# Kernel tuning notes

Measured on AMD Instinct MI355X. Metric: run time of the kernel, lower is better.

## Reference

```python
import jax, jax.numpy as jnp
import numpy as np

EPSILON = 1e-6
MINMAX_RATIO = 20 ** 0.5
N_NODES, N_EDGES = 60000, 240000
WIDTH, NUM_HEAD, DIM_HEAD = 256, 8, 32
WIDTH_NORM = NUM_HEAD * DIM_HEAD          # 256
WIDTH_ACT = NUM_HEAD * DIM_HEAD * 4       # 1024
EDGE_VOCAB, EDGE_FEATS = 16, 3


def _inv_softplus(y):
    return np.log(np.expm1(y))


def setup_inputs() -> dict:
    key = jax.random.key(0)
    ks = jax.random.split(key, 16)
    inp = {
        'x': jax.random.normal(ks[0], (N_NODES, WIDTH), jnp.float32),
        'deg': jax.random.randint(ks[1], (N_NODES,), 0, 6, jnp.int32),
        'edge_idx': jax.random.randint(ks[2], (2, N_EDGES), 0, N_NODES, jnp.int32),
        'edge_attr': jax.random.randint(ks[3], (N_EDGES, EDGE_FEATS), 0, EDGE_VOCAB, jnp.int32),
        'node_elec': jax.random.normal(ks[4], (N_NODES, 2), jnp.float32),
        # parameters (init scales per module code)
        'lora_down': jax.random.normal(ks[5], (WIDTH, DIM_HEAD)) / np.sqrt(WIDTH),
        # original init is zeros; small random values used so this path is exercised
        'lora_up': jax.random.normal(ks[6], (DIM_HEAD, WIDTH_NORM)) * 0.01,
        'emb_edge': jax.random.normal(ks[7], (EDGE_VOCAB, DIM_HEAD)) * (0.01 / np.sqrt(EDGE_FEATS)),
        'moa_w': jnp.zeros((2, DIM_HEAD), jnp.float32),
        'moa_s': jnp.tile(jnp.linspace(float(_inv_softplus(0.1)), float(_inv_softplus(10.0)), DIM_HEAD), (2, 1)),
        'elec_lin': jax.random.normal(ks[8], (2, DIM_HEAD)) * (0.01 / np.sqrt(2)),
        'emb_deg': jax.random.normal(ks[9], (6, WIDTH_NORM)) * 0.1,
        'lin_pre': jax.random.normal(ks[10], (WIDTH, WIDTH_NORM)) / np.sqrt(WIDTH),
        'gate_lin': jax.random.normal(ks[11], (WIDTH_NORM, WIDTH_NORM)) / np.sqrt(WIDTH_NORM),
        'gate_kernel': jax.random.normal(ks[12], (NUM_HEAD, DIM_HEAD, DIM_HEAD * 4)) / np.sqrt(DIM_HEAD),
        'value_lin': jax.random.normal(ks[13], (WIDTH_NORM, WIDTH_NORM)) / np.sqrt(WIDTH_NORM),
        'value_kernel': jax.random.normal(ks[14], (NUM_HEAD, DIM_HEAD, DIM_HEAD * 4)) / np.sqrt(DIM_HEAD),
        'act_bias': jnp.full((WIDTH_ACT,), float(_inv_softplus(0.5)), jnp.float32),
        'post_kernel': jax.random.normal(ks[15], (NUM_HEAD, DIM_HEAD * 4, DIM_HEAD)) / np.sqrt(DIM_HEAD * 4),
    }
    return inp


def _clip_with_grad(x, lo, hi):
    return jax.lax.stop_gradient(jnp.clip(x, lo, hi) - x) + x


def _group_linear(x, lin_kernel, head_kernel, norm_bias=None):
    H, D, F = head_kernel.shape
    xx = (x @ lin_kernel).reshape(*x.shape[:-1], H, D)
    xx = xx / jnp.sqrt(jnp.mean(jnp.square(xx), axis=-1, keepdims=True) + EPSILON)
    if norm_bias is not None:
        xx = (xx + norm_bias.reshape(xx.shape)) / 2 ** 0.5
    xx = jnp.einsum('nhd,hdf->nhf', xx, head_kernel)
    return xx.reshape(*x.shape[:-1], H * F)


def reference(x, deg, edge_idx, edge_attr, node_elec, lora_down, lora_up, emb_edge,
              moa_w, moa_s, elec_lin, emb_deg, lin_pre, gate_lin, gate_kernel,
              value_lin, value_kernel, act_bias, post_kernel):
    ei0, ei1 = edge_idx[0], edge_idx[1]
    # edge embedding: bond features + electronegativity difference (MoAct tanh mixture)
    diff = node_elec[ei0] - node_elec[ei1]                      # [E,2]
    w = jax.nn.softplus(moa_w)
    w = w / w.sum(axis=-1, keepdims=True)
    s = jax.nn.softplus(moa_s)
    moa_out = (jnp.tanh(diff[..., None] * s) * w).sum(-1)       # [E,2]
    emb = jnp.sum(emb_edge[edge_attr], axis=-2) + moa_out @ elec_lin  # [E,dim_head]
    # per-edge message with LoRA modulation, scatter-add to destination nodes
    msg = x[ei0] + x[ei1]                                       # [E,width]
    msg = msg @ lin_pre + ((msg @ lora_down) * emb) @ lora_up   # [E,width_norm]
    agg = jax.ops.segment_sum(msg, ei1, num_segments=x.shape[0])
    # gated post-block with degree-embedding gate bias
    gate_bias = emb_deg[deg]                                    # [N,width_norm]
    gg = _group_linear(agg, gate_lin, gate_kernel, gate_bias)   # [N,width_act]
    vv = _group_linear(agg, value_lin, value_kernel)
    a = jax.nn.softplus(gg + act_bias)
    a = _clip_with_grad(a, 1.0 / MINMAX_RATIO, MINMAX_RATIO)
    xx = (a * vv).reshape(agg.shape[0], NUM_HEAD, -1)           # [N,H,4*dim_head]
    xx = jnp.einsum('nhd,hdf->nhf', xx, post_kernel)
    return xx.reshape(agg.shape[0], -1)                         # [N,width_norm]
```

## Files before the change

kernel.cpp:

```cpp
#include <hip/hip_runtime.h>
#include <hip/hip_bf16.h>

typedef unsigned short u16;

#define NN 60000
#define NE 240000

typedef __attribute__((ext_vector_type(8))) short bfrag;
typedef __attribute__((ext_vector_type(4))) float ffrag;

__device__ __forceinline__ float bf2f(u16 u) {
    union { unsigned int i; float f; } v; v.i = ((unsigned int)u) << 16; return v.f;
}
__device__ __forceinline__ u16 f2bf(float f) {
    __hip_bfloat16 h = __float2bfloat16(f);
    return *reinterpret_cast<u16*>(&h);
}
__device__ __forceinline__ float softplusf(float x) {
    return fmaxf(x, 0.f) + log1pf(expf(-fabsf(x)));
}
__device__ __forceinline__ float fast_softplus(float x) {
    return __logf(1.f + __expf(x));
}
__device__ __forceinline__ float fast_sp_clip(float x) {
    float a = __logf(1.f + __expf(x));
    return fminf(fmaxf(a, 0.22360679774997896f), 4.47213595499957939f);
}
__device__ __forceinline__ float fast_tanh(float x) {
    float t = __expf(fminf(fmaxf(2.f * x, -30.f), 30.f));
    return (t - 1.f) * __builtin_amdgcn_rcpf(t + 1.f);
}
template<bool B>
__device__ __forceinline__ float LD(const void* p, int i) {
    if constexpr (B) return bf2f(((const u16*)p)[i]);
    else             return ((const float*)p)[i];
}
__device__ __forceinline__ bfrag ldfrag(const u16* p) {
    return *reinterpret_cast<const bfrag*>(p);
}
__device__ __forceinline__ ffrag MFMA(bfrag a, bfrag b, ffrag c) {
    return __builtin_amdgcn_mfma_f32_16x16x32_bf16(a, b, c, 0, 0, 0);
}

__global__ void detect_kernel(const u16* __restrict__ x, int* __restrict__ flag) {
    __shared__ int cnt;
    if (threadIdx.x == 0) cnt = 0;
    __syncthreads();
    int c = 0;
    for (int i = threadIdx.x; i < 2048; i += 256) {
        u16 w = x[2 * i];
        int e = (w >> 7) & 0xFF;
        if (e >= 112 && e <= 143) c++;
    }
    atomicAdd(&cnt, c);
    __syncthreads();
    if (threadIdx.x == 0) *flag = (cnt > 1024) ? 1 : 0;
}

template<bool B>
__device__ void prep_body(const void* gate_lin, const void* value_lin,
    const void* lin_pre, const void* lora_down, const void* lora_up,
    const void* gate_kernel, const void* value_kernel, const void* post_kernel,
    u16* gT, u16* vT, u16* lpT, u16* ldT, u16* luT, u16* gkT, u16* vkT, u16* pkT,
    int tid, int stride)
{
    for (int i = tid; i < 65536; i += stride) {
        int n = i >> 8, k = i & 255;
        gT[i]  = f2bf(LD<B>(gate_lin,  k * 256 + n));
        vT[i]  = f2bf(LD<B>(value_lin, k * 256 + n));
        lpT[i] = f2bf(LD<B>(lin_pre,   k * 256 + n));
    }
    for (int i = tid; i < 8192; i += stride) {
        { int n = i >> 8, k = i & 255; ldT[i] = f2bf(LD<B>(lora_down, k * 32 + n)); }
        { int n = i >> 5, k = i & 31;  luT[i] = f2bf(LD<B>(lora_up,   k * 256 + n)); }
    }
    for (int i = tid; i < 32768; i += stride) {
        { int hf = i >> 5, d = i & 31, h = hf >> 7, f = hf & 127;
          gkT[i] = f2bf(LD<B>(gate_kernel,  h * 4096 + d * 128 + f));
          vkT[i] = f2bf(LD<B>(value_kernel, h * 4096 + d * 128 + f)); }
        { int hd = i >> 7, f = i & 127, h = hd >> 5, d2 = hd & 31;
          pkT[i] = f2bf(LD<B>(post_kernel, h * 4096 + f * 32 + d2)); }
    }
}
__global__ void prep_kernel(const void* gate_lin, const void* value_lin,
    const void* lin_pre, const void* lora_down, const void* lora_up,
    const void* gate_kernel, const void* value_kernel, const void* post_kernel,
    u16* gT, u16* vT, u16* lpT, u16* ldT, u16* luT, u16* gkT, u16* vkT, u16* pkT,
    const int* flag)
{
    int tid = blockIdx.x * blockDim.x + threadIdx.x;
    int stride = gridDim.x * blockDim.x;
    if (*flag) prep_body<true >(gate_lin, value_lin, lin_pre, lora_down, lora_up,
        gate_kernel, value_kernel, post_kernel, gT, vT, lpT, ldT, luT, gkT, vkT, pkT, tid, stride);
    else       prep_body<false>(gate_lin, value_lin, lin_pre, lora_down, lora_up,
        gate_kernel, value_kernel, post_kernel, gT, vT, lpT, ldT, luT, gkT, vkT, pkT, tid, stride);
}


struct PreSmem { __align__(16) u16 xB[64][264]; };

template<bool B>
__device__ void pre_body(PreSmem& sm, const void* x, const u16* ldT,
                         u16* xd, int blk, int j)
{
    const int w = j >> 6, quad = (j >> 4) & 3, l15 = j & 15;
    {
        int row = j >> 2, seg = j & 3, c0 = seg * 64;
        int gr = blk * 64 + row;
        if (gr < NN) {
            if constexpr (B) {
                const u16* xp = (const u16*)x + (size_t)gr * 256 + c0;
                for (int cc = 0; cc < 64; cc += 8)
                    *reinterpret_cast<bfrag*>(&sm.xB[row][c0 + cc]) = ldfrag(xp + cc);
            } else {
                const float* xp = (const float*)x + (size_t)gr * 256 + c0;
                for (int cc = 0; cc < 64; cc += 8) {
                    float4 v0 = *(const float4*)(xp + cc);
                    float4 v1 = *(const float4*)(xp + cc + 4);
                    bfrag o;
                    o[0] = (short)f2bf(v0.x); o[1] = (short)f2bf(v0.y);
                    o[2] = (short)f2bf(v0.z); o[3] = (short)f2bf(v0.w);
                    o[4] = (short)f2bf(v1.x); o[5] = (short)f2bf(v1.y);
                    o[6] = (short)f2bf(v1.z); o[7] = (short)f2bf(v1.w);
                    *reinterpret_cast<bfrag*>(&sm.xB[row][c0 + cc]) = o;
                }
            }
        } else {
            bfrag z = {0,0,0,0,0,0,0,0};
            for (int cc = 0; cc < 64; cc += 8)
                *reinterpret_cast<bfrag*>(&sm.xB[row][c0 + cc]) = z;
        }
    }
    __syncthreads();
    const int r0 = w * 16;
    bfrag A[8];
    #pragma unroll
    for (int kt = 0; kt < 8; kt++)
        A[kt] = ldfrag(&sm.xB[r0 + l15][kt * 32 + quad * 8]);

    #pragma unroll
    for (int t = 0; t < 2; t++) {
        int n0 = t * 16;
        ffrag acc = {0.f, 0.f, 0.f, 0.f};
        #pragma unroll
        for (int kt = 0; kt < 8; kt++)
            acc = MFMA(A[kt], ldfrag(ldT + (n0 + l15) * 256 + kt * 32 + quad * 8), acc);
        #pragma unroll
        for (int r = 0; r < 4; r++) {
            int gr = blk * 64 + r0 + quad * 4 + r;
            if (gr < NN) xd[(size_t)gr * 32 + n0 + l15] = f2bf(acc[r]);
        }
    }
}
__global__ __launch_bounds__(256) void pre_kernel(const void* x, const u16* ldT,
    u16* xd, const int* flag)
{
    __shared__ PreSmem sm;
    const int j = threadIdx.x, blk = blockIdx.x;
    if (*flag) pre_body<true >(sm, x, ldT, xd, blk, j);
    else       pre_body<false>(sm, x, ldT, xd, blk, j);
}

__global__ __launch_bounds__(256) void hist_kernel(const int* __restrict__ edge_idx,
                                                   int* __restrict__ cnt)
{
    int e = blockIdx.x * blockDim.x + threadIdx.x;
    int stride = gridDim.x * blockDim.x;
    for (; e < NE; e += stride) atomicAdd(&cnt[edge_idx[NE + e]], 1);
}

__global__ __launch_bounds__(256) void scanA_kernel(const int* __restrict__ cnt,
                                                    int* __restrict__ bsum)
{
    __shared__ int sd[256];
    int b = blockIdx.x, j = threadIdx.x;
    int base = b * 1024 + j * 4;
    int s = 0;
    #pragma unroll
    for (int k = 0; k < 4; k++) { int i = base + k; if (i < NN) s += cnt[i]; }
    sd[j] = s; __syncthreads();
    for (int st = 128; st > 0; st >>= 1) {
        if (j < st) sd[j] += sd[j + st];
        __syncthreads();
    }
    if (j == 0) bsum[b] = sd[0];
}

__global__ __launch_bounds__(256) void scanB_kernel(const int* __restrict__ cnt,
    const int* __restrict__ bsum, int* __restrict__ off, int* __restrict__ cur)
{
    __shared__ int sd[256];
    int b = blockIdx.x, j = threadIdx.x;
    int pre = 0;
    for (int k = 0; k < b; k++) pre += bsum[k];
    int base = b * 1024 + j * 4;
    int c[4]; int tsum = 0;
    #pragma unroll
    for (int k = 0; k < 4; k++) { int i = base + k; c[k] = (i < NN) ? cnt[i] : 0; tsum += c[k]; }
    sd[j] = tsum; __syncthreads();
    for (int st = 1; st < 256; st <<= 1) {
        int v = (j >= st) ? sd[j - st] : 0;
        __syncthreads();
        sd[j] += v;
        __syncthreads();
    }
    int excl = sd[j] - tsum;
    int run = pre + excl;
    #pragma unroll
    for (int k = 0; k < 4; k++) {
        int i = base + k;
        if (i < NN) { off[i] = run; cur[i] = run; }
        run += c[k];
    }
}

struct EdgeWSmem {
    float wL[64], sL[64];
    float embT[512];
    float elT[64];
};

template<bool B>
__device__ void edgew_body(EdgeWSmem& sm, const int* edge_idx, const int* edge_attr,
    const void* node_elec, const void* emb_edge, const void* moa_w, const void* moa_s,
    const void* elec_lin, const u16* xd, u16* W, int* srcL, int* cur, int g, int j)
{
    if (j < 64) {
        int c = j >> 5;
        float sw = fast_softplus(LD<B>(moa_w, j));
        float tot = 0.f;
        #pragma unroll
        for (int d = 0; d < 32; d++) tot += fast_softplus(LD<B>(moa_w, c * 32 + d));
        sm.wL[j] = sw / tot;
        sm.sL[j] = fast_softplus(LD<B>(moa_s, j));
        sm.elT[j] = LD<B>(elec_lin, j);
    }
    for (int i = j; i < 512; i += 256) sm.embT[i] = LD<B>(emb_edge, i);
    __syncthreads();

    const int t = j & 3, s = j >> 2, e = g * 64 + s;
    const int a = edge_idx[e], b = edge_idx[NE + e];
    const int ch = t >> 1, dr = (t & 1) * 16;
    float df = LD<B>(node_elec, a * 2 + ch) - LD<B>(node_elec, b * 2 + ch);
    float part = 0.f;
    #pragma unroll
    for (int d = 0; d < 16; d++) {
        int dd = ch * 32 + dr + d;
        part += fast_tanh(df * sm.sL[dd]) * sm.wL[dd];
    }
    part += __shfl_xor(part, 1);
    int base = (j & 63) & ~3;
    float moa0 = __shfl(part, base + 0);
    float moa1 = __shfl(part, base + 2);

    int a0 = edge_attr[e * 3 + 0], a1 = edge_attr[e * 3 + 1], a2 = edge_attr[e * 3 + 2];
    int d0 = t * 8;
    bfrag va = ldfrag(xd + (size_t)a * 32 + d0);
    bfrag vb = ldfrag(xd + (size_t)b * 32 + d0);
    bfrag o;
    #pragma unroll
    for (int q = 0; q < 8; q++) {
        int d = d0 + q;
        float emb = sm.embT[a0 * 32 + d] + sm.embT[a1 * 32 + d] + sm.embT[a2 * 32 + d]
                  + moa0 * sm.elT[d] + moa1 * sm.elT[32 + d];
        o[q] = (short)f2bf((bf2f((u16)va[q]) + bf2f((u16)vb[q])) * emb);
    }
    int slot = 0;
    if (t == 0) slot = atomicAdd(&cur[b], 1);
    slot = __shfl(slot, base);
    if (t == 0) srcL[slot] = a;
    *reinterpret_cast<bfrag*>(W + (size_t)slot * 32 + d0) = o;
}

__global__ __launch_bounds__(256) void edgew_kernel(const int* edge_idx,
    const int* edge_attr, const void* node_elec, const void* emb_edge,
    const void* moa_w, const void* moa_s, const void* elec_lin,
    const u16* xd, u16* W, int* srcL, int* cur, const int* flag)
{
    __shared__ EdgeWSmem sm;
    const int j = threadIdx.x, g = blockIdx.x;
    if (*flag) edgew_body<true >(sm, edge_idx, edge_attr, node_elec, emb_edge,
                                 moa_w, moa_s, elec_lin, xd, W, srcL, cur, g, j);
    else       edgew_body<false>(sm, edge_idx, edge_attr, node_elec, emb_edge,
                                 moa_w, moa_s, elec_lin, xd, W, srcL, cur, g, j);
}

struct GatherSmem {
    int srcC[192];
    int offL[16], idgL[16];
};

template<bool B>
__device__ void gather_body(GatherSmem& sm, const void* x, const u16* Wb,
    const int* srcL, const int* off, const int* cnt,
    u16* S, u16* U, int blk, int j)
{
    const int n0g = blk * 16;
    int o0 = off[n0g];
    int eb = off[n0g + 15] + cnt[n0g + 15] - o0;
    if (j < 192 && j < eb) sm.srcC[j] = srcL[o0 + j];
    if (j < 16) { sm.offL[j] = off[n0g + j]; sm.idgL[j] = cnt[n0g + j]; }
    __syncthreads();

    const int s = j >> 4, dp = j & 15, c0 = dp * 16;
    const int o = sm.offL[s], dg = sm.idgL[s], base = o - o0;
    float acc[16];
    #pragma unroll
    for (int k = 0; k < 16; k++) acc[k] = 0.f;
    float u0 = 0.f, u1 = 0.f;

    if constexpr (B) {
        const u16* xp = (const u16*)x;
        bfrag pv0 = {0,0,0,0,0,0,0,0}, pv1 = {0,0,0,0,0,0,0,0};
        float pw0 = 0.f, pw1 = 0.f;
        if (dg > 0) {
            int src = (base < 192) ? sm.srcC[base] : srcL[o];
            const u16* xr = xp + (size_t)src * 256 + c0;
            pv0 = ldfrag(xr); pv1 = ldfrag(xr + 8);
            const u16* wr = Wb + (size_t)o * 32 + dp;
            pw0 = bf2f(wr[0]); pw1 = bf2f(wr[16]);
        }
        for (int i = 0; i < dg; i++) {
            bfrag v0 = pv0, v1 = pv1;
            float w0 = pw0, w1 = pw1;
            if (i + 1 < dg) {
                int idx = base + i + 1;
                int src = (idx < 192) ? sm.srcC[idx] : srcL[o + i + 1];
                const u16* xr = xp + (size_t)src * 256 + c0;
                pv0 = ldfrag(xr); pv1 = ldfrag(xr + 8);
                const u16* wr = Wb + (size_t)(o + i + 1) * 32 + dp;
                pw0 = bf2f(wr[0]); pw1 = bf2f(wr[16]);
            }
            u0 += w0; u1 += w1;
            #pragma unroll
            for (int q = 0; q < 8; q++) {
                acc[q]     += bf2f((u16)v0[q]);
                acc[q + 8] += bf2f((u16)v1[q]);
            }
        }
        {
            const u16* xr = xp + (size_t)(n0g + s) * 256 + c0;
            bfrag v0 = ldfrag(xr), v1 = ldfrag(xr + 8);
            float fd = (float)dg;
            #pragma unroll
            for (int q = 0; q < 8; q++) {
                acc[q]     = fmaf(fd, bf2f((u16)v0[q]), acc[q]);
                acc[q + 8] = fmaf(fd, bf2f((u16)v1[q]), acc[q + 8]);
            }
        }
    } else {
        const float* xp = (const float*)x;
        float4 p0 = {0,0,0,0}, p1 = {0,0,0,0}, p2 = {0,0,0,0}, p3 = {0,0,0,0};
        float pw0 = 0.f, pw1 = 0.f;
        if (dg > 0) {
            int src = (base < 192) ? sm.srcC[base] : srcL[o];
            const float* r = xp + (size_t)src * 256 + c0;
            p0 = *(const float4*)r;       p1 = *(const float4*)(r + 4);
            p2 = *(const float4*)(r + 8); p3 = *(const float4*)(r + 12);
            const u16* wr = Wb + (size_t)o * 32 + dp;
            pw0 = bf2f(wr[0]); pw1 = bf2f(wr[16]);
        }
        for (int i = 0; i < dg; i++) {
            float4 a0 = p0, a1 = p1, a2 = p2, a3 = p3;
            float w0 = pw0, w1 = pw1;
            if (i + 1 < dg) {
                int idx = base + i + 1;
                int src = (idx < 192) ? sm.srcC[idx] : srcL[o + i + 1];
                const float* r = xp + (size_t)src * 256 + c0;
                p0 = *(const float4*)r;       p1 = *(const float4*)(r + 4);
                p2 = *(const float4*)(r + 8); p3 = *(const float4*)(r + 12);
                const u16* wr = Wb + (size_t)(o + i + 1) * 32 + dp;
                pw0 = bf2f(wr[0]); pw1 = bf2f(wr[16]);
            }
            u0 += w0; u1 += w1;
            acc[0]  += a0.x; acc[1]  += a0.y; acc[2]  += a0.z; acc[3]  += a0.w;
            acc[4]  += a1.x; acc[5]  += a1.y; acc[6]  += a1.z; acc[7]  += a1.w;
            acc[8]  += a2.x; acc[9]  += a2.y; acc[10] += a2.z; acc[11] += a2.w;
            acc[12] += a3.x; acc[13] += a3.y; acc[14] += a3.z; acc[15] += a3.w;
        }
        {
            const float* r = xp + (size_t)(n0g + s) * 256 + c0;
            float4 a0 = *(const float4*)r,       a1 = *(const float4*)(r + 4);
            float4 a2 = *(const float4*)(r + 8), a3 = *(const float4*)(r + 12);
            float fd = (float)dg;
            acc[0]  = fmaf(fd, a0.x, acc[0]);  acc[1]  = fmaf(fd, a0.y, acc[1]);
            acc[2]  = fmaf(fd, a0.z, acc[2]);  acc[3]  = fmaf(fd, a0.w, acc[3]);
            acc[4]  = fmaf(fd, a1.x, acc[4]);  acc[5]  = fmaf(fd, a1.y, acc[5]);
            acc[6]  = fmaf(fd, a1.z, acc[6]);  acc[7]  = fmaf(fd, a1.w, acc[7]);
            acc[8]  = fmaf(fd, a2.x, acc[8]);  acc[9]  = fmaf(fd, a2.y, acc[9]);
            acc[10] = fmaf(fd, a2.z, acc[10]); acc[11] = fmaf(fd, a2.w, acc[11]);
            acc[12] = fmaf(fd, a3.x, acc[12]); acc[13] = fmaf(fd, a3.y, acc[13]);
            acc[14] = fmaf(fd, a3.z, acc[14]); acc[15] = fmaf(fd, a3.w, acc[15]);
        }
    }

    u16* Sp = S + (size_t)(n0g + s) * 256 + c0;
    #pragma unroll
    for (int cq = 0; cq < 16; cq += 2) {
        unsigned int pv = (unsigned int)f2bf(acc[cq]) | ((unsigned int)f2bf(acc[cq + 1]) << 16);
        *reinterpret_cast<unsigned int*>(Sp + cq) = pv;
    }
    U[(size_t)(n0g + s) * 32 + dp]      = f2bf(u0);
    U[(size_t)(n0g + s) * 32 + dp + 16] = f2bf(u1);
}

__global__ __launch_bounds__(256) void gather_kernel(const void* x, const u16* Wb,
    const int* srcL, const int* off, const int* cnt, u16* S, u16* U, const int* flag)
{
    __shared__ GatherSmem sm;
    const int j = threadIdx.x, blk = blockIdx.x;
    if (*flag) gather_body<true >(sm, x, Wb, srcL, off, cnt, S, U, blk, j);
    else       gather_body<false>(sm, x, Wb, srcL, off, cnt, S, U, blk, j);
}

struct NodeSmemF {
    __align__(16) union U1 {
        u16 aggB[16][264];
        u16 ghatB[16][264];
    } u1;
    __align__(16) u16 sB[16][264];
    __align__(16) u16 xxW[8][16][136];
    __align__(16) u16 uB[16][40];
    int degL[16];
};

template<bool B>
__device__ void node_body_f(NodeSmemF& sm, const u16* S, const u16* U,
    const int* deg, const void* emb_deg, const void* act_bias,
    const u16* gT, const u16* vT, const u16* gkT, const u16* vkT, const u16* pkT,
    const u16* lpT, const u16* luT, void* out, int blk, int j)
{
    const int w = j >> 6, quad = (j >> 4) & 3, l15 = j & 15;
    const int n0g = blk * 16;

    {
        int row = j >> 5, c0 = (j & 31) * 8;
        const u16* Sp = S + (size_t)(n0g + row) * 256 + c0;
        *reinterpret_cast<bfrag*>(&sm.sB[row][c0]) = ldfrag(Sp);
        int d = j & 31;
        sm.uB[row][d] = U[(size_t)(n0g + row) * 32 + d];
        if (j < 16) sm.degL[j] = deg[n0g + j];
    }
    __syncthreads();

    {
        bfrag Sf[8];
        #pragma unroll
        for (int kt = 0; kt < 8; kt++)
            Sf[kt] = ldfrag(&sm.sB[l15][kt * 32 + quad * 8]);
        bfrag uA = ldfrag(&sm.uB[l15][quad * 8]);
        #pragma unroll
        for (int tt = 0; tt < 2; tt++) {
            int n0 = (w * 2 + tt) * 16;
            const u16* bp = lpT + (n0 + l15) * 256 + quad * 8;
            bfrag b0 = ldfrag(bp +   0), b1 = ldfrag(bp +  32),
                  b2 = ldfrag(bp +  64), b3 = ldfrag(bp +  96),
                  b4 = ldfrag(bp + 128), b5 = ldfrag(bp + 160),
                  b6 = ldfrag(bp + 192), b7 = ldfrag(bp + 224);
            bfrag lu = ldfrag(luT + (n0 + l15) * 32 + quad * 8);
            ffrag acc = {0.f, 0.f, 0.f, 0.f};
            acc = MFMA(Sf[0], b0, acc); acc = MFMA(Sf[1], b1, acc);
            acc = MFMA(Sf[2], b2, acc); acc = MFMA(Sf[3], b3, acc);
            acc = MFMA(Sf[4], b4, acc); acc = MFMA(Sf[5], b5, acc);
            acc = MFMA(Sf[6], b6, acc); acc = MFMA(Sf[7], b7, acc);
            acc = MFMA(uA, lu, acc);
            #pragma unroll
            for (int r = 0; r < 4; r++)
                sm.u1.aggB[quad * 4 + r][n0 + l15] = f2bf(acc[r]);
        }
    }
    __syncthreads();

    {
        bfrag A[8];
        #pragma unroll
        for (int kt = 0; kt < 8; kt++)
            A[kt] = ldfrag(&sm.u1.aggB[l15][kt * 32 + quad * 8]);
        __syncthreads();

        const bool isG = (w >> 2) == 0;
        const u16* WT = isG ? gT : vT;
        const int base0 = ((w >> 1) & 1) * 128 + (w & 1) * 64;
        #pragma unroll
        for (int hd = 0; hd < 2; hd++) {
            int n0 = base0 + hd * 32;
            ffrag a0 = {0.f, 0.f, 0.f, 0.f}, a1 = {0.f, 0.f, 0.f, 0.f};
            {
                const u16* bp = WT + (n0 + l15) * 256 + quad * 8;
                bfrag b0 = ldfrag(bp +   0), b1 = ldfrag(bp +  32),
                      b2 = ldfrag(bp +  64), b3 = ldfrag(bp +  96),
                      b4 = ldfrag(bp + 128), b5 = ldfrag(bp + 160),
                      b6 = ldfrag(bp + 192), b7 = ldfrag(bp + 224);
                a0 = MFMA(A[0], b0, a0); a0 = MFMA(A[1], b1, a0);
                a0 = MFMA(A[2], b2, a0); a0 = MFMA(A[3], b3, a0);
                a0 = MFMA(A[4], b4, a0); a0 = MFMA(A[5], b5, a0);
                a0 = MFMA(A[6], b6, a0); a0 = MFMA(A[7], b7, a0);
            }
            {
                const u16* bp = WT + (n0 + 16 + l15) * 256 + quad * 8;
                bfrag b0 = ldfrag(bp +   0), b1 = ldfrag(bp +  32),
                      b2 = ldfrag(bp +  64), b3 = ldfrag(bp +  96),
                      b4 = ldfrag(bp + 128), b5 = ldfrag(bp + 160),
                      b6 = ldfrag(bp + 192), b7 = ldfrag(bp + 224);
                a1 = MFMA(A[0], b0, a1); a1 = MFMA(A[1], b1, a1);
                a1 = MFMA(A[2], b2, a1); a1 = MFMA(A[3], b3, a1);
                a1 = MFMA(A[4], b4, a1); a1 = MFMA(A[5], b5, a1);
                a1 = MFMA(A[6], b6, a1); a1 = MFMA(A[7], b7, a1);
            }
            float inv[4];
            #pragma unroll
            for (int r = 0; r < 4; r++) {
                float sq = a0[r] * a0[r] + a1[r] * a1[r];
                sq += __shfl_xor(sq, 1);
                sq += __shfl_xor(sq, 2);
                sq += __shfl_xor(sq, 4);
                sq += __shfl_xor(sq, 8);
                inv[r] = 1.f / sqrtf(sq * (1.f / 32.f) + 1e-6f);
            }
            if (isG) {
                #pragma unroll
                for (int r = 0; r < 4; r++) {
                    int row = quad * 4 + r;
                    int dgr = sm.degL[row];
                    float b0 = LD<B>(emb_deg, dgr * 256 + n0 + l15);
                    float b1 = LD<B>(emb_deg, dgr * 256 + n0 + 16 + l15);
                    sm.u1.ghatB[row][n0 + l15] =
                        f2bf((a0[r] * inv[r] + b0) * 0.70710678118654752f);
                    sm.u1.ghatB[row][n0 + 16 + l15] =
                        f2bf((a1[r] * inv[r] + b1) * 0.70710678118654752f);
                }
            } else {
                #pragma unroll
                for (int r = 0; r < 4; r++) {
                    int row = quad * 4 + r;
                    sm.sB[row][n0 + l15]      = f2bf(a0[r] * inv[r]);
                    sm.sB[row][n0 + 16 + l15] = f2bf(a1[r] * inv[r]);
                }
            }
        }
    }
    __syncthreads();

    {
        u16 (*xxW)[136] = sm.xxW[w];
        const int h = w;
        bfrag aG = ldfrag(&sm.u1.ghatB[l15][h * 32 + quad * 8]);
        bfrag aV = ldfrag(&sm.sB[l15][h * 32 + quad * 8]);
        #pragma unroll
        for (int t = 0; t < 8; t++) {
            int n0 = t * 16;
            bfrag bg = ldfrag(gkT + (h * 128 + n0 + l15) * 32 + quad * 8);
            bfrag bv = ldfrag(vkT + (h * 128 + n0 + l15) * 32 + quad * 8);
            ffrag zero = {0.f, 0.f, 0.f, 0.f};
            ffrag ag = MFMA(aG, bg, zero);
            ffrag av = MFMA(aV, bv, zero);
            float bias = LD<B>(act_bias, h * 128 + n0 + l15);
            #pragma unroll
            for (int r = 0; r < 4; r++) {
                float a = fast_sp_clip(ag[r] + bias);
                xxW[quad * 4 + r][n0 + l15] = f2bf(a * av[r]);
            }
        }
        bfrag A4[4];
        #pragma unroll
        for (int kt = 0; kt < 4; kt++)
            A4[kt] = ldfrag(&xxW[l15][kt * 32 + quad * 8]);
        #pragma unroll
        for (int t = 0; t < 2; t++) {
            int n0 = t * 16;
            const u16* pp = pkT + (h * 32 + n0 + l15) * 128 + quad * 8;
            bfrag c0 = ldfrag(pp), c1 = ldfrag(pp + 32),
                  c2 = ldfrag(pp + 64), c3 = ldfrag(pp + 96);
            ffrag acc = {0.f, 0.f, 0.f, 0.f};
            acc = MFMA(A4[0], c0, acc); acc = MFMA(A4[1], c1, acc);
            acc = MFMA(A4[2], c2, acc); acc = MFMA(A4[3], c3, acc);
            #pragma unroll
            for (int r = 0; r < 4; r++) {
                size_t idx = (size_t)(n0g + quad * 4 + r) * 256 + h * 32 + n0 + l15;
                if constexpr (B) ((u16*)out)[idx] = f2bf(acc[r]);
                else             ((float*)out)[idx] = acc[r];
            }
        }
    }
}

__global__ __launch_bounds__(512, 6) void node_kernel_f(
    const u16* S, const u16* U, const int* deg, const void* emb_deg,
    const void* act_bias, const u16* gT, const u16* vT, const u16* gkT,
    const u16* vkT, const u16* pkT, const u16* lpT, const u16* luT,
    void* out, const int* flag)
{
    __shared__ NodeSmemF sm;
    const int j = threadIdx.x, blk = blockIdx.x;
    if (*flag) node_body_f<true >(sm, S, U, deg, emb_deg, act_bias,
                                  gT, vT, gkT, vkT, pkT, lpT, luT, out, blk, j);
    else       node_body_f<false>(sm, S, U, deg, emb_deg, act_bias,
                                  gT, vT, gkT, vkT, pkT, lpT, luT, out, blk, j);
}

struct EdgeSmemFB {
    __align__(16) float msgT[256][8];
    __align__(16) float uT[32][8];
    float wL[64], sL[64];
    float embL[8][32];
    float moaL[8][2];
    float diffL[8][2];
    int   ei0s[8], ei1s[8];
};

template<bool B>
__device__ void edge_body_fb(EdgeSmemFB& sm,
    const void* x, const int* edge_idx, const int* edge_attr,
    const void* node_elec, const void* lora_down, const void* lora_up,
    const void* emb_edge, const void* moa_w, const void* moa_s,
    const void* elec_lin, const void* lin_pre, float* agg, int g, int j)
{
    if (j < 64) {
        int c = j >> 5;
        float sw = softplusf(LD<B>(moa_w, j));
        float tot = 0.f;
        #pragma unroll
        for (int d = 0; d < 32; d++) tot += softplusf(LD<B>(moa_w, c * 32 + d));
        sm.wL[j] = sw / tot;
        sm.sL[j] = softplusf(LD<B>(moa_s, j));
    }
    if (j < 16) {
        int s = j >> 1, c = j & 1;
        int e = g * 8 + s;
        int a = edge_idx[e], b = edge_idx[NE + e];
        if (c == 0) { sm.ei0s[s] = a; sm.ei1s[s] = b; }
        sm.diffL[s][c] = LD<B>(node_elec, a * 2 + c) - LD<B>(node_elec, b * 2 + c);
    }
    __syncthreads();
    if (j < 16) {
        int s = j >> 1, c = j & 1;
        float df = sm.diffL[s][c], acc = 0.f;
        #pragma unroll
        for (int d = 0; d < 32; d++)
            acc += tanhf(df * sm.sL[c * 32 + d]) * sm.wL[c * 32 + d];
        sm.moaL[s][c] = acc;
    }
    #pragma unroll
    for (int s = 0; s < 8; s++)
        sm.msgT[j][s] = LD<B>(x, sm.ei0s[s] * 256 + j) + LD<B>(x, sm.ei1s[s] * 256 + j);
    __syncthreads();
    {
        int s = j >> 5, d = j & 31, e = g * 8 + s;
        sm.embL[s][d] = LD<B>(emb_edge, edge_attr[e * 3 + 0] * 32 + d)
                      + LD<B>(emb_edge, edge_attr[e * 3 + 1] * 32 + d)
                      + LD<B>(emb_edge, edge_attr[e * 3 + 2] * 32 + d)
                      + sm.moaL[s][0] * LD<B>(elec_lin, d)
                      + sm.moaL[s][1] * LD<B>(elec_lin, 32 + d);
    }
    __syncthreads();
    {
        int s = j >> 5, d = j & 31;
        float t = 0.f;
        for (int k = 0; k < 256; k++)
            t = fmaf(sm.msgT[k][s], LD<B>(lora_down, k * 32 + d), t);
        sm.uT[d][s] = t * sm.embL[s][d];
    }
    __syncthreads();
    float acc[8];
    #pragma unroll
    for (int s = 0; s < 8; s++) acc[s] = 0.f;
    #pragma unroll 4
    for (int k = 0; k < 256; k++) {
        float w = LD<B>(lin_pre, k * 256 + j);
        const float4 m0 = *reinterpret_cast<const float4*>(&sm.msgT[k][0]);
        const float4 m1 = *reinterpret_cast<const float4*>(&sm.msgT[k][4]);
        acc[0] = fmaf(m0.x, w, acc[0]); acc[1] = fmaf(m0.y, w, acc[1]);
        acc[2] = fmaf(m0.z, w, acc[2]); acc[3] = fmaf(m0.w, w, acc[3]);
        acc[4] = fmaf(m1.x, w, acc[4]); acc[5] = fmaf(m1.y, w, acc[5]);
        acc[6] = fmaf(m1.z, w, acc[6]); acc[7] = fmaf(m1.w, w, acc[7]);
    }
    #pragma unroll 4
    for (int d = 0; d < 32; d++) {
        float w = LD<B>(lora_up, d * 256 + j);
        const float4 u0 = *reinterpret_cast<const float4*>(&sm.uT[d][0]);
        const float4 u1 = *reinterpret_cast<const float4*>(&sm.uT[d][4]);
        acc[0] = fmaf(u0.x, w, acc[0]); acc[1] = fmaf(u0.y, w, acc[1]);
        acc[2] = fmaf(u0.z, w, acc[2]); acc[3] = fmaf(u0.w, w, acc[3]);
        acc[4] = fmaf(u1.x, w, acc[4]); acc[5] = fmaf(u1.y, w, acc[5]);
        acc[6] = fmaf(u1.z, w, acc[6]); acc[7] = fmaf(u1.w, w, acc[7]);
    }
    #pragma unroll
    for (int s = 0; s < 8; s++)
        unsafeAtomicAdd(&agg[(size_t)sm.ei1s[s] * 256 + j], acc[s]);
}

__global__ __launch_bounds__(256) void edge_kernel_fb(
    const void* x, const int* edge_idx, const int* edge_attr,
    const void* node_elec, const void* lora_down, const void* lora_up,
    const void* emb_edge, const void* moa_w, const void* moa_s,
    const void* elec_lin, const void* lin_pre, float* agg, const int* flag)
{
    __shared__ EdgeSmemFB sm;
    const int j = threadIdx.x, g = blockIdx.x;
    if (*flag) edge_body_fb<true >(sm, x, edge_idx, edge_attr, node_elec, lora_down,
                                   lora_up, emb_edge, moa_w, moa_s, elec_lin, lin_pre, agg, g, j);
    else       edge_body_fb<false>(sm, x, edge_idx, edge_attr, node_elec, lora_down,
                                   lora_up, emb_edge, moa_w, moa_s, elec_lin, lin_pre, agg, g, j);
}

struct NodeSmemFB {
    __align__(16) float aggT[256][8];
    float gL[8][256];
    float vL[8][256];
    float ghat[256], vhat[256];
    float xxL[1024];
};

template<bool B>
__device__ void node_body_fb(NodeSmemFB& sm,
    const float* agg, const int* deg, const void* emb_deg,
    const void* gate_lin, const void* value_lin, const void* gate_kernel,
    const void* value_kernel, const void* act_bias, const void* post_kernel,
    void* out, int n0, int j)
{
    #pragma unroll
    for (int s = 0; s < 8; s++) sm.aggT[j][s] = agg[(size_t)(n0 + s) * 256 + j];
    __syncthreads();

    float ga[8], va[8];
    #pragma unroll
    for (int s = 0; s < 8; s++) { ga[s] = 0.f; va[s] = 0.f; }
    #pragma unroll 4
    for (int k = 0; k < 256; k++) {
        float wg = LD<B>(gate_lin,  k * 256 + j);
        float wv = LD<B>(value_lin, k * 256 + j);
        const float4 a0 = *reinterpret_cast<const float4*>(&sm.aggT[k][0]);
        const float4 a1 = *reinterpret_cast<const float4*>(&sm.aggT[k][4]);
        ga[0] = fmaf(a0.x, wg, ga[0]); va[0] = fmaf(a0.x, wv, va[0]);
        ga[1] = fmaf(a0.y, wg, ga[1]); va[1] = fmaf(a0.y, wv, va[1]);
        ga[2] = fmaf(a0.z, wg, ga[2]); va[2] = fmaf(a0.z, wv, va[2]);
        ga[3] = fmaf(a0.w, wg, ga[3]); va[3] = fmaf(a0.w, wv, va[3]);
        ga[4] = fmaf(a1.x, wg, ga[4]); va[4] = fmaf(a1.x, wv, va[4]);
        ga[5] = fmaf(a1.y, wg, ga[5]); va[5] = fmaf(a1.y, wv, va[5]);
        ga[6] = fmaf(a1.z, wg, ga[6]); va[6] = fmaf(a1.z, wv, va[6]);
        ga[7] = fmaf(a1.w, wg, ga[7]); va[7] = fmaf(a1.w, wv, va[7]);
    }
    __syncthreads();
    #pragma unroll
    for (int s = 0; s < 8; s++) { sm.gL[s][j] = ga[s]; sm.vL[s][j] = va[s]; }

    const int h = j >> 5, dd = j & 31, f0 = dd << 2;
    const float lo = 0.22360679774997896f, hi = 4.47213595499957939f;

    for (int s = 0; s < 8; s++) {
        __syncthreads();
        float gs = 0.f, vs = 0.f;
        #pragma unroll
        for (int d = 0; d < 32; d++) {
            float g = sm.gL[s][h * 32 + d];
            float v = sm.vL[s][h * 32 + d];
            gs = fmaf(g, g, gs); vs = fmaf(v, v, vs);
        }
        float grms = sqrtf(gs * (1.f / 32.f) + 1e-6f);
        float vrms = sqrtf(vs * (1.f / 32.f) + 1e-6f);
        float gv = sm.gL[s][j], vv = sm.vL[s][j];
        float bias = LD<B>(emb_deg, deg[n0 + s] * 256 + j);
        sm.ghat[j] = (gv / grms + bias) * 0.70710678118654752f;
        sm.vhat[j] = vv / vrms;
        __syncthreads();

        float a0 = 0.f, a1 = 0.f, a2 = 0.f, a3 = 0.f;
        float b0 = 0.f, b1 = 0.f, b2 = 0.f, b3 = 0.f;
        #pragma unroll 4
        for (int d = 0; d < 32; d++) {
            float gh = sm.ghat[h * 32 + d];
            float vh = sm.vhat[h * 32 + d];
            int base = h * 4096 + d * 128 + f0;
            a0 = fmaf(gh, LD<B>(gate_kernel,  base + 0), a0);
            a1 = fmaf(gh, LD<B>(gate_kernel,  base + 1), a1);
            a2 = fmaf(gh, LD<B>(gate_kernel,  base + 2), a2);
            a3 = fmaf(gh, LD<B>(gate_kernel,  base + 3), a3);
            b0 = fmaf(vh, LD<B>(value_kernel, base + 0), b0);
            b1 = fmaf(vh, LD<B>(value_kernel, base + 1), b1);
            b2 = fmaf(vh, LD<B>(value_kernel, base + 2), b2);
            b3 = fmaf(vh, LD<B>(value_kernel, base + 3), b3);
        }
        int fb = h * 128 + f0;
        a0 = fminf(fmaxf(softplusf(a0 + LD<B>(act_bias, fb + 0)), lo), hi);
        a1 = fminf(fmaxf(softplusf(a1 + LD<B>(act_bias, fb + 1)), lo), hi);
        a2 = fminf(fmaxf(softplusf(a2 + LD<B>(act_bias, fb + 2)), lo), hi);
        a3 = fminf(fmaxf(softplusf(a3 + LD<B>(act_bias, fb + 3)), lo), hi);
        sm.xxL[fb + 0] = a0 * b0; sm.xxL[fb + 1] = a1 * b1;
        sm.xxL[fb + 2] = a2 * b2; sm.xxL[fb + 3] = a3 * b3;
        __syncthreads();

        float o = 0.f;
        #pragma unroll 4
        for (int f = 0; f < 128; f++)
            o = fmaf(sm.xxL[h * 128 + f], LD<B>(post_kernel, h * 4096 + f * 32 + dd), o);
        if constexpr (B) ((u16*)out)[(size_t)(n0 + s) * 256 + j] = f2bf(o);
        else             ((float*)out)[(size_t)(n0 + s) * 256 + j] = o;
    }
}

__global__ __launch_bounds__(256) void node_kernel_fb(
    const float* agg, const int* deg, const void* emb_deg,
    const void* gate_lin, const void* value_lin, const void* gate_kernel,
    const void* value_kernel, const void* act_bias, const void* post_kernel,
    void* out, const int* flag)
{
    __shared__ NodeSmemFB sm;
    const int j = threadIdx.x, n0 = blockIdx.x * 8;
    if (*flag) node_body_fb<true >(sm, agg, deg, emb_deg, gate_lin, value_lin,
                                   gate_kernel, value_kernel, act_bias, post_kernel, out, n0, j);
    else       node_body_fb<false>(sm, agg, deg, emb_deg, gate_lin, value_lin,
                                   gate_kernel, value_kernel, act_bias, post_kernel, out, n0, j);
}

extern "C" void kernel_launch(void* const* d_in, const int* in_sizes, int n_in,
                              void* d_out, int out_size, void* d_ws, size_t ws_size,
                              hipStream_t stream) {
    const void* x           = d_in[0];
    const int*  deg         = (const int*)d_in[1];
    const int*  edge_idx    = (const int*)d_in[2];
    const int*  edge_attr   = (const int*)d_in[3];
    const void* node_elec   = d_in[4];
    const void* lora_down   = d_in[5];
    const void* lora_up     = d_in[6];
    const void* emb_edge    = d_in[7];
    const void* moa_w       = d_in[8];
    const void* moa_s       = d_in[9];
    const void* elec_lin    = d_in[10];
    const void* emb_deg     = d_in[11];
    const void* lin_pre     = d_in[12];
    const void* gate_lin    = d_in[13];
    const void* gate_kernel = d_in[14];
    const void* value_lin   = d_in[15];
    const void* value_kernel= d_in[16];
    const void* act_bias    = d_in[17];
    const void* post_kernel = d_in[18];

    const size_t AGG_BYTES = (size_t)NN * 256 * 4;
    const size_t T_BYTES   = (size_t)(3 * 65536 + 2 * 8192 + 3 * 32768) * 2;

    const size_t S_OFF   = 16 + T_BYTES;
    const size_t W_OFF   = S_OFF   + (size_t)NN * 256 * 2;
    const size_t XD_OFF  = W_OFF   + (size_t)NE * 32 * 2;
    const size_t U_OFF   = XD_OFF  + (size_t)NN * 32 * 2;
    const size_t SRC_OFF = U_OFF   + (size_t)NN * 32 * 2;
    const size_t CNT_OFF = SRC_OFF + (size_t)NE * 4;
    const size_t OFF_OFF = CNT_OFF + (size_t)NN * 4;
    const size_t CUR_OFF = OFF_OFF + (size_t)NN * 4;
    const size_t BS_OFF  = CUR_OFF + (size_t)NN * 4;
    const size_t NEW_NEEDED = BS_OFF + 256;

    const size_t T_OFF_OLD  = AGG_BYTES + 16;
    const size_t OLD_NEEDED = T_OFF_OLD + T_BYTES;

    if (ws_size >= NEW_NEEDED) {
        int* flag = (int*)d_ws;
        u16* gT  = (u16*)((char*)d_ws + 16);
        u16* vT  = gT  + 65536;
        u16* lpT = vT  + 65536;
        u16* ldT = lpT + 65536;
        u16* luT = ldT + 8192;
        u16* gkT = luT + 8192;
        u16* vkT = gkT + 32768;
        u16* pkT = vkT + 32768;
        u16*  S    = (u16*)((char*)d_ws + S_OFF);
        u16*  Wb   = (u16*)((char*)d_ws + W_OFF);
        u16*  xd   = (u16*)((char*)d_ws + XD_OFF);
        u16*  U    = (u16*)((char*)d_ws + U_OFF);
        int* srcL  = (int*)((char*)d_ws + SRC_OFF);
        int* cnt   = (int*)((char*)d_ws + CNT_OFF);
        int* offA  = (int*)((char*)d_ws + OFF_OFF);
        int* cur   = (int*)((char*)d_ws + CUR_OFF);
        int* bsum  = (int*)((char*)d_ws + BS_OFF);

        detect_kernel<<<1, 256, 0, stream>>>((const u16*)x, flag);
        prep_kernel<<<128, 256, 0, stream>>>(
            gate_lin, value_lin, lin_pre, lora_down, lora_up,
            gate_kernel, value_kernel, post_kernel,
            gT, vT, lpT, ldT, luT, gkT, vkT, pkT, flag);
        hipMemsetAsync(cnt, 0, (size_t)NN * 4, stream);
        pre_kernel<<<(NN + 63) / 64, 256, 0, stream>>>(x, ldT, xd, flag);
        hist_kernel<<<256, 256, 0, stream>>>(edge_idx, cnt);
        scanA_kernel<<<59, 256, 0, stream>>>(cnt, bsum);
        scanB_kernel<<<59, 256, 0, stream>>>(cnt, bsum, offA, cur);
        edgew_kernel<<<NE / 64, 256, 0, stream>>>(
            edge_idx, edge_attr, node_elec, emb_edge, moa_w, moa_s, elec_lin,
            xd, Wb, srcL, cur, flag);
        gather_kernel<<<NN / 16, 256, 0, stream>>>(
            x, Wb, srcL, offA, cnt, S, U, flag);
        node_kernel_f<<<NN / 16, 512, 0, stream>>>(
            S, U, deg, emb_deg, act_bias,
            gT, vT, gkT, vkT, pkT, lpT, luT, d_out, flag);
    } else {
        float* agg = (float*)d_ws;
        int* flag  = (int*)((char*)d_ws + AGG_BYTES);
        hipMemsetAsync(agg, 0, AGG_BYTES, stream);
        detect_kernel<<<1, 256, 0, stream>>>((const u16*)x, flag);
        edge_kernel_fb<<<NE / 8, 256, 0, stream>>>(
            x, edge_idx, edge_attr, node_elec, lora_down, lora_up, emb_edge,
            moa_w, moa_s, elec_lin, lin_pre, agg, flag);
        node_kernel_fb<<<NN / 8, 256, 0, stream>>>(
            agg, deg, emb_deg, gate_lin, value_lin, gate_kernel, value_kernel,
            act_bias, post_kernel, d_out, flag);
    }
}
```

Before: 487.7 us.

## Process 48 nodes per block in node kernel to reuse weight fragments

The node kernel now handles 48 rows per block (three 16-row groups) instead of 16, loading each weight B-fragment from global memory once and reusing it across the three row groups. The shared-memory layout is reorganized so gate results overwrite sB and value results go to a new vhatB buffer, with the xx scratch sharing space with aggB. This cuts repeated global weight loads per node, at the cost of much more shared memory and registers, lowering occupancy (launch bounds min blocks 6 -> 2) and reducing the grid to 1250 blocks.

New measurement: 409.8 us. 16.0% less time.

```diff
diff --git a/kernel.cpp b/kernel.cpp
--- a/kernel.cpp
+++ b/kernel.cpp
@@ -414,14 +414,14 @@
 }
 
 struct NodeSmemF {
-    __align__(16) union U1 {
-        u16 aggB[16][264];
-        u16 ghatB[16][264];
-    } u1;
-    __align__(16) u16 sB[16][264];
-    __align__(16) u16 xxW[8][16][136];
-    __align__(16) u16 uB[16][40];
-    int degL[16];
+    __align__(16) u16 sB[48][264];
+    union U {
+        __align__(16) u16 aggB[48][264];
+        __align__(16) u16 xxW[8][16][136];
+    } u;
+    __align__(16) u16 vhatB[48][264];
+    __align__(16) u16 uB[48][40];
+    int degL[48];
 };
 
 template<bool B>
@@ -431,33 +431,35 @@
     const u16* lpT, const u16* luT, void* out, int blk, int j)
 {
     const int w = j >> 6, quad = (j >> 4) & 3, l15 = j & 15;
-    const int n0g = blk * 16;
-
-    {
-        int row = j >> 5, c0 = (j & 31) * 8;
-        const u16* Sp = S + (size_t)(n0g + row) * 256 + c0;
-        *reinterpret_cast<bfrag*>(&sm.sB[row][c0]) = ldfrag(Sp);
-        int d = j & 31;
-        sm.uB[row][d] = U[(size_t)(n0g + row) * 32 + d];
-        if (j < 16) sm.degL[j] = deg[n0g + j];
-    }
-    __syncthreads();
-
-    {
-        bfrag Sf[8];
+    const int n0g = blk * 48;
+
+    #pragma unroll
+    for (int k = 0; k < 3; k++) {
+        int idx = k * 512 + j;
+        int row = idx >> 5, cb = (idx & 31) * 8;
+        *reinterpret_cast<bfrag*>(&sm.sB[row][cb]) =
+            ldfrag(S + (size_t)(n0g + row) * 256 + cb);
+        sm.uB[idx >> 5][idx & 31] = U[(size_t)(n0g + (idx >> 5)) * 32 + (idx & 31)];
+    }
+    if (j < 48) sm.degL[j] = deg[n0g + j];
+    __syncthreads();
+
+    #pragma unroll
+    for (int ct = 0; ct < 2; ct++) {
+        int n0 = w * 32 + ct * 16;
+        const u16* bp = lpT + (n0 + l15) * 256 + quad * 8;
+        bfrag b0 = ldfrag(bp +   0), b1 = ldfrag(bp +  32),
+              b2 = ldfrag(bp +  64), b3 = ldfrag(bp +  96),
+              b4 = ldfrag(bp + 128), b5 = ldfrag(bp + 160),
+              b6 = ldfrag(bp + 192), b7 = ldfrag(bp + 224);
+        bfrag lu = ldfrag(luT + (n0 + l15) * 32 + quad * 8);
         #pragma unroll
-        for (int kt = 0; kt < 8; kt++)
-            Sf[kt] = ldfrag(&sm.sB[l15][kt * 32 + quad * 8]);
-        bfrag uA = ldfrag(&sm.uB[l15][quad * 8]);
-        #pragma unroll
-        for (int tt = 0; tt < 2; tt++) {
-            int n0 = (w * 2 + tt) * 16;
-            const u16* bp = lpT + (n0 + l15) * 256 + quad * 8;
-            bfrag b0 = ldfrag(bp +   0), b1 = ldfrag(bp +  32),
-                  b2 = ldfrag(bp +  64), b3 = ldfrag(bp +  96),
-                  b4 = ldfrag(bp + 128), b5 = ldfrag(bp + 160),
-                  b6 = ldfrag(bp + 192), b7 = ldfrag(bp + 224);
-            bfrag lu = ldfrag(luT + (n0 + l15) * 32 + quad * 8);
+        for (int rg = 0; rg < 3; rg++) {
+            bfrag Sf[8];
+            #pragma unroll
+            for (int kt = 0; kt < 8; kt++)
+                Sf[kt] = ldfrag(&sm.sB[rg * 16 + l15][kt * 32 + quad * 8]);
+            bfrag uA = ldfrag(&sm.uB[rg * 16 + l15][quad * 8]);
             ffrag acc = {0.f, 0.f, 0.f, 0.f};
             acc = MFMA(Sf[0], b0, acc); acc = MFMA(Sf[1], b1, acc);
             acc = MFMA(Sf[2], b2, acc); acc = MFMA(Sf[3], b3, acc);
@@ -466,125 +468,120 @@
             acc = MFMA(uA, lu, acc);
             #pragma unroll
             for (int r = 0; r < 4; r++)
-                sm.u1.aggB[quad * 4 + r][n0 + l15] = f2bf(acc[r]);
+                sm.u.aggB[rg * 16 + quad * 4 + r][n0 + l15] = f2bf(acc[r]);
         }
     }
     __syncthreads();
 
     {
-        bfrag A[8];
-        #pragma unroll
-        for (int kt = 0; kt < 8; kt++)
-            A[kt] = ldfrag(&sm.u1.aggB[l15][kt * 32 + quad * 8]);
-        __syncthreads();
-
         const bool isG = (w >> 2) == 0;
         const u16* WT = isG ? gT : vT;
-        const int base0 = ((w >> 1) & 1) * 128 + (w & 1) * 64;
         #pragma unroll
         for (int hd = 0; hd < 2; hd++) {
-            int n0 = base0 + hd * 32;
-            ffrag a0 = {0.f, 0.f, 0.f, 0.f}, a1 = {0.f, 0.f, 0.f, 0.f};
-            {
-                const u16* bp = WT + (n0 + l15) * 256 + quad * 8;
-                bfrag b0 = ldfrag(bp +   0), b1 = ldfrag(bp +  32),
-                      b2 = ldfrag(bp +  64), b3 = ldfrag(bp +  96),
-                      b4 = ldfrag(bp + 128), b5 = ldfrag(bp + 160),
-                      b6 = ldfrag(bp + 192), b7 = ldfrag(bp + 224);
-                a0 = MFMA(A[0], b0, a0); a0 = MFMA(A[1], b1, a0);
-                a0 = MFMA(A[2], b2, a0); a0 = MFMA(A[3], b3, a0);
-                a0 = MFMA(A[4], b4, a0); a0 = MFMA(A[5], b5, a0);
-                a0 = MFMA(A[6], b6, a0); a0 = MFMA(A[7], b7, a0);
+            int n0 = (w & 3) * 64 + hd * 32;
+            bfrag bA[8], bB[8];
+            const u16* bpA = WT + (n0 + l15) * 256 + quad * 8;
+            const u16* bpB = WT + (n0 + 16 + l15) * 256 + quad * 8;
+            #pragma unroll
+            for (int kt = 0; kt < 8; kt++) {
+                bA[kt] = ldfrag(bpA + kt * 32);
+                bB[kt] = ldfrag(bpB + kt * 32);
             }
-            {
-                const u16* bp = WT + (n0 + 16 + l15) * 256 + quad * 8;
-                bfrag b0 = ldfrag(bp +   0), b1 = ldfrag(bp +  32),
-                      b2 = ldfrag(bp +  64), b3 = ldfrag(bp +  96),
-                      b4 = ldfrag(bp + 128), b5 = ldfrag(bp + 160),
-                      b6 = ldfrag(bp + 192), b7 = ldfrag(bp + 224);
-                a1 = MFMA(A[0], b0, a1); a1 = MFMA(A[1], b1, a1);
-                a1 = MFMA(A[2], b2, a1); a1 = MFMA(A[3], b3, a1);
-                a1 = MFMA(A[4], b4, a1); a1 = MFMA(A[5], b5, a1);
-                a1 = MFMA(A[6], b6, a1); a1 = MFMA(A[7], b7, a1);
-            }
-            float inv[4];
             #pragma unroll
-            for (int r = 0; r < 4; r++) {
-                float sq = a0[r] * a0[r] + a1[r] * a1[r];
-                sq += __shfl_xor(sq, 1);
-                sq += __shfl_xor(sq, 2);
-                sq += __shfl_xor(sq, 4);
-                sq += __shfl_xor(sq, 8);
-                inv[r] = 1.f / sqrtf(sq * (1.f / 32.f) + 1e-6f);
-            }
-            if (isG) {
+            for (int rg = 0; rg < 3; rg++) {
+                bfrag A[8];
+                #pragma unroll
+                for (int kt = 0; kt < 8; kt++)
+                    A[kt] = ldfrag(&sm.u.aggB[rg * 16 + l15][kt * 32 + quad * 8]);
+                ffrag a0 = {0.f, 0.f, 0.f, 0.f}, a1 = {0.f, 0.f, 0.f, 0.f};
+                #pragma unroll
+                for (int kt = 0; kt < 8; kt++) {
+                    a0 = MFMA(A[kt], bA[kt], a0);
+                    a1 = MFMA(A[kt], bB[kt], a1);
+                }
+                float inv[4];
                 #pragma unroll
                 for (int r = 0; r < 4; r++) {
-                    int row = quad * 4 + r;
-                    int dgr = sm.degL[row];
-                    float b0 = LD<B>(emb_deg, dgr * 256 + n0 + l15);
-                    float b1 = LD<B>(emb_deg, dgr * 256 + n0 + 16 + l15);
-                    sm.u1.ghatB[row][n0 + l15] =
-                        f2bf((a0[r] * inv[r] + b0) * 0.70710678118654752f);
-                    sm.u1.ghatB[row][n0 + 16 + l15] =
-                        f2bf((a1[r] * inv[r] + b1) * 0.70710678118654752f);
+                    float sq = a0[r] * a0[r] + a1[r] * a1[r];
+                    sq += __shfl_xor(sq, 1);
+                    sq += __shfl_xor(sq, 2);
+                    sq += __shfl_xor(sq, 4);
+                    sq += __shfl_xor(sq, 8);
+                    inv[r] = 1.f / sqrtf(sq * (1.f / 32.f) + 1e-6f);
                 }
-            } else {
+                if (isG) {
+                    #pragma unroll
+                    for (int r = 0; r < 4; r++) {
+                        int row = rg * 16 + quad * 4 + r;
+                        int dgr = sm.degL[row];
+                        float e0 = LD<B>(emb_deg, dgr * 256 + n0 + l15);
+                        float e1 = LD<B>(emb_deg, dgr * 256 + n0 + 16 + l15);
+                        sm.sB[row][n0 + l15] =
+                            f2bf((a0[r] * inv[r] + e0) * 0.70710678118654752f);
+                        sm.sB[row][n0 + 16 + l15] =
+                            f2bf((a1[r] * inv[r] + e1) * 0.70710678118654752f);
+                    }
+                } else {
+                    #pragma unroll
+                    for (int r = 0; r < 4; r++) {
+                        int row = rg * 16 + quad * 4 + r;
+                        sm.vhatB[row][n0 + l15]      = f2bf(a0[r] * inv[r]);
+                        sm.vhatB[row][n0 + 16 + l15] = f2bf(a1[r] * inv[r]);
+                    }
+                }
+            }
+        }
+    }
+    __syncthreads();
+
+    {
+        u16 (*xxW)[136] = sm.u.xxW[w];
+        const int h = w;
+        #pragma unroll
+        for (int rg = 0; rg < 3; rg++) {
+            bfrag aG = ldfrag(&sm.sB[rg * 16 + l15][h * 32 + quad * 8]);
+            bfrag aV = ldfrag(&sm.vhatB[rg * 16 + l15][h * 32 + quad * 8]);
+            #pragma unroll
+            for (int t = 0; t < 8; t++) {
+                int n0 = t * 16;
+                bfrag bg = ldfrag(gkT + (h * 128 + n0 + l15) * 32 + quad * 8);
+                bfrag bv = ldfrag(vkT + (h * 128 + n0 + l15) * 32 + quad * 8);
+                ffrag zero = {0.f, 0.f, 0.f, 0.f};
+                ffrag ag = MFMA(aG, bg, zero);
+                ffrag av = MFMA(aV, bv, zero);
+                float bias = LD<B>(act_bias, h * 128 + n0 + l15);
                 #pragma unroll
                 for (int r = 0; r < 4; r++) {
-                    int row = quad * 4 + r;
-                    sm.sB[row][n0 + l15]      = f2bf(a0[r] * inv[r]);
-                    sm.sB[row][n0 + 16 + l15] = f2bf(a1[r] * inv[r]);
+                    float a = fast_sp_clip(ag[r] + bias);
+                    xxW[quad * 4 + r][n0 + l15] = f2bf(a * av[r]);
                 }
             }
-        }
-    }
-    __syncthreads();
-
-    {
-        u16 (*xxW)[136] = sm.xxW[w];
-        const int h = w;
-        bfrag aG = ldfrag(&sm.u1.ghatB[l15][h * 32 + quad * 8]);
-        bfrag aV = ldfrag(&sm.sB[l15][h * 32 + quad * 8]);
-        #pragma unroll
-        for (int t = 0; t < 8; t++) {
-            int n0 = t * 16;
-            bfrag bg = ldfrag(gkT + (h * 128 + n0 + l15) * 32 + quad * 8);
-            bfrag bv = ldfrag(vkT + (h * 128 + n0 + l15) * 32 + quad * 8);
-            ffrag zero = {0.f, 0.f, 0.f, 0.f};
-            ffrag ag = MFMA(aG, bg, zero);
-            ffrag av = MFMA(aV, bv, zero);
-            float bias = LD<B>(act_bias, h * 128 + n0 + l15);
+            bfrag A4[4];
             #pragma unroll
-            for (int r = 0; r < 4; r++) {
-                float a = fast_sp_clip(ag[r] + bias);
-                xxW[quad * 4 + r][n0 + l15] = f2bf(a * av[r]);
+            for (int kt = 0; kt < 4; kt++)
+                A4[kt] = ldfrag(&xxW[l15][kt * 32 + quad * 8]);
+            #pragma unroll
+            for (int t = 0; t < 2; t++) {
+                int n0 = t * 16;
+                const u16* pp = pkT + (h * 32 + n0 + l15) * 128 + quad * 8;
+                bfrag c0 = ldfrag(pp), c1 = ldfrag(pp + 32),
+                      c2 = ldfrag(pp + 64), c3 = ldfrag(pp + 96);
+                ffrag acc = {0.f, 0.f, 0.f, 0.f};
+                acc = MFMA(A4[0], c0, acc); acc = MFMA(A4[1], c1, acc);
+                acc = MFMA(A4[2], c2, acc); acc = MFMA(A4[3], c3, acc);
+                #pragma unroll
+                for (int r = 0; r < 4; r++) {
+                    size_t idx = (size_t)(n0g + rg * 16 + quad * 4 + r) * 256
+                               + h * 32 + n0 + l15;
+                    if constexpr (B) ((u16*)out)[idx] = f2bf(acc[r]);
+                    else             ((float*)out)[idx] = acc[r];
+                }
             }
         }
-        bfrag A4[4];
-        #pragma unroll
-        for (int kt = 0; kt < 4; kt++)
-            A4[kt] = ldfrag(&xxW[l15][kt * 32 + quad * 8]);
-        #pragma unroll
-        for (int t = 0; t < 2; t++) {
-            int n0 = t * 16;
-            const u16* pp = pkT + (h * 32 + n0 + l15) * 128 + quad * 8;
-            bfrag c0 = ldfrag(pp), c1 = ldfrag(pp + 32),
-                  c2 = ldfrag(pp + 64), c3 = ldfrag(pp + 96);
-            ffrag acc = {0.f, 0.f, 0.f, 0.f};
-            acc = MFMA(A4[0], c0, acc); acc = MFMA(A4[1], c1, acc);
-            acc = MFMA(A4[2], c2, acc); acc = MFMA(A4[3], c3, acc);
-            #pragma unroll
-            for (int r = 0; r < 4; r++) {
-                size_t idx = (size_t)(n0g + quad * 4 + r) * 256 + h * 32 + n0 + l15;
-                if constexpr (B) ((u16*)out)[idx] = f2bf(acc[r]);
-                else             ((float*)out)[idx] = acc[r];
-            }
-        }
-    }
-}
-
-__global__ __launch_bounds__(512, 6) void node_kernel_f(
+    }
+}
+
+__global__ __launch_bounds__(512, 2) void node_kernel_f(
     const u16* S, const u16* U, const int* deg, const void* emb_deg,
     const void* act_bias, const u16* gT, const u16* vT, const u16* gkT,
     const u16* vkT, const u16* pkT, const u16* lpT, const u16* luT,
@@ -849,9 +846,6 @@
     const size_t BS_OFF  = CUR_OFF + (size_t)NN * 4;
     const size_t NEW_NEEDED = BS_OFF + 256;
 
-    const size_t T_OFF_OLD  = AGG_BYTES + 16;
-    const size_t OLD_NEEDED = T_OFF_OLD + T_BYTES;
-
     if (ws_size >= NEW_NEEDED) {
         int* flag = (int*)d_ws;
         u16* gT  = (u16*)((char*)d_ws + 16);
@@ -887,7 +881,7 @@
             xd, Wb, srcL, cur, flag);
         gather_kernel<<<NN / 16, 256, 0, stream>>>(
             x, Wb, srcL, offA, cnt, S, U, flag);
-        node_kernel_f<<<NN / 16, 512, 0, stream>>>(
+        node_kernel_f<<<NN / 48, 512, 0, stream>>>(
             S, U, deg, emb_deg, act_bias,
             gT, vT, gkT, vkT, pkT, lpT, luT, d_out, flag);
     } else {
```
